# Optimization experiments

Measured on AMD Instinct MI355X. Metric: run time of the kernel, lower is better.

## Reference

```python
import jax, jax.numpy as jnp
import numpy as np

CH = 128; HEADS = 4; HD = CH // HEADS; L = 4; G = 16; NPG = 1024
N = G * NPG; E = 524288; IN_DIM = 64; BN_EPS = 1e-5


def setup_inputs() -> dict:
    key = jax.random.key(0)
    ks = iter(jax.random.split(key, 64))
    def nrm(shape, scale):
        return jax.random.normal(next(ks), shape, dtype=jnp.float32) * scale
    inp = {}
    inp['x'] = jax.random.normal(next(ks), (N, IN_DIM), dtype=jnp.float32)
    inp['edge_attr'] = jnp.ones((E, 1), dtype=jnp.float32)
    inp['edge_index'] = jax.random.randint(next(ks), (2, E), 0, N)
    inp['batch'] = jnp.repeat(jnp.arange(G), NPG)  # equal-sized graphs, sorted
    # input projections
    inp['node_w'] = nrm((CH, IN_DIM), IN_DIM ** -0.5); inp['node_b'] = nrm((CH,), 0.02)
    inp['edge_w'] = nrm((CH, 1), 1.0); inp['edge_b'] = nrm((CH,), 0.02)
    # per-layer stacked params
    inp['gine_w1'] = nrm((L, CH, CH), CH ** -0.5); inp['gine_b1'] = nrm((L, CH), 0.02)
    inp['gine_w2'] = nrm((L, CH, CH), CH ** -0.5); inp['gine_b2'] = nrm((L, CH), 0.02)
    inp['attn_in_w'] = nrm((L, 3 * CH, CH), CH ** -0.5); inp['attn_in_b'] = nrm((L, 3 * CH), 0.02)
    inp['attn_out_w'] = nrm((L, CH, CH), CH ** -0.5); inp['attn_out_b'] = nrm((L, CH), 0.02)
    inp['mlp_w1'] = nrm((L, 2 * CH, CH), CH ** -0.5); inp['mlp_b1'] = nrm((L, 2 * CH), 0.02)
    inp['mlp_w2'] = nrm((L, CH, 2 * CH), (2 * CH) ** -0.5); inp['mlp_b2'] = nrm((L, CH), 0.02)
    # 3 batch norms per layer (eval mode: running stats)
    inp['bn_g'] = 1.0 + nrm((L, 3, CH), 0.05)
    inp['bn_b'] = nrm((L, 3, CH), 0.05)
    inp['bn_m'] = nrm((L, 3, CH), 0.05)
    inp['bn_v'] = 0.5 + jax.random.uniform(next(ks), (L, 3, CH), dtype=jnp.float32)
    # head MLP 128 -> 64 -> 32 -> 1
    inp['head_w1'] = nrm((64, CH), CH ** -0.5); inp['head_b1'] = nrm((64,), 0.02)
    inp['head_w2'] = nrm((32, 64), 64 ** -0.5); inp['head_b2'] = nrm((32,), 0.02)
    inp['head_w3'] = nrm((1, 32), 32 ** -0.5); inp['head_b3'] = nrm((1,), 0.02)
    return inp


def _bn(h, g, b, m, v):
    return (h - m) * jax.lax.rsqrt(v + BN_EPS) * g + b


def _mha(x, in_w, in_b, out_w, out_b):
    # x: [G, NPG, CH]; torch.nn.MultiheadAttention self-attention, no padding (full graphs)
    qkv = x @ in_w.T + in_b
    q, k, v = jnp.split(qkv, 3, axis=-1)
    split = lambda t: t.reshape(G, NPG, HEADS, HD).transpose(0, 2, 1, 3)
    q, k, v = split(q), split(k), split(v)
    scores = jnp.einsum('ghid,ghjd->ghij', q, k) / jnp.sqrt(jnp.float32(HD))
    a = jax.nn.softmax(scores, axis=-1)
    o = jnp.einsum('ghij,ghjd->ghid', a, v).transpose(0, 2, 1, 3).reshape(G, NPG, CH)
    return o @ out_w.T + out_b


def reference(x, edge_attr, edge_index, batch, node_w, node_b, edge_w, edge_b,
              gine_w1, gine_b1, gine_w2, gine_b2,
              attn_in_w, attn_in_b, attn_out_w, attn_out_b,
              mlp_w1, mlp_b1, mlp_w2, mlp_b2,
              bn_g, bn_b, bn_m, bn_v,
              head_w1, head_b1, head_w2, head_b2, head_w3, head_b3):
    h = x @ node_w.T + node_b                      # [N, CH]
    e = edge_attr @ edge_w.T + edge_b              # [E, CH]
    src, dst = edge_index[0], edge_index[1]
    for l in range(L):
        # --- GINEConv: nn((1+eps)*x_i + sum_j relu(x_j + e_ji)), eps=0 ---
        msg = jax.nn.relu(h[src] + e)
        agg = jax.ops.segment_sum(msg, dst, num_segments=N)
        z = h + agg
        z = jax.nn.relu(z @ gine_w1[l].T + gine_b1[l]) @ gine_w2[l].T + gine_b2[l]
        h1 = _bn(z + h, bn_g[l, 0], bn_b[l, 0], bn_m[l, 0], bn_v[l, 0])
        # --- global multihead attention on dense batch of x ---
        a = _mha(h.reshape(G, NPG, CH), attn_in_w[l], attn_in_b[l],
                 attn_out_w[l], attn_out_b[l]).reshape(N, CH)
        h2 = _bn(a + h, bn_g[l, 1], bn_b[l, 1], bn_m[l, 1], bn_v[l, 1])
        # --- combine + FFN (GPSConv mlp: CH -> 2CH -> CH) ---
        out = h1 + h2
        ff = jax.nn.relu(out @ mlp_w1[l].T + mlp_b1[l]) @ mlp_w2[l].T + mlp_b2[l]
        h = _bn(out + ff, bn_g[l, 2], bn_b[l, 2], bn_m[l, 2], bn_v[l, 2])
    # global_add_pool + head MLP
    g = jax.ops.segment_sum(h, batch, num_segments=G)
    g = jax.nn.relu(g @ head_w1.T + head_b1)
    g = jax.nn.relu(g @ head_w2.T + head_b2)
    return g @ head_w3.T + head_b3
```

## Files before the change

### kernel.cpp

```cpp
#include <hip/hip_runtime.h>
#include <hip/hip_bf16.h>

typedef __attribute__((ext_vector_type(8))) short short8;
typedef __attribute__((ext_vector_type(4))) float f32x4;
typedef __attribute__((ext_vector_type(2))) unsigned int u32x2;
typedef unsigned short u16;
typedef unsigned int u32;
typedef unsigned long long u64;

#define NODES 16384
#define CHN 128
#define NEDGE 524288
#define NG 16
#define NPGC 1024
#define NHEAD 4
#define HDIM 32
#define NLAYER 4
#define CL 0.2550348281f

#if __has_builtin(__builtin_amdgcn_exp2f)
#define EXP2(x) __builtin_amdgcn_exp2f(x)
#else
#define EXP2(x) exp2f(x)
#endif

__device__ __forceinline__ float bf2f(u16 u) {
    union { u32 u; float f; } c; c.u = ((u32)u) << 16; return c.f;
}
__device__ __forceinline__ u16 f2bf(float f) {
    union { float f; u32 u; } c; c.f = f;
    u32 r = c.u + 0x7fffu + ((c.u >> 16) & 1u);
    return (u16)(r >> 16);
}
__device__ __forceinline__ void fsplit(float f, u16& hi, u16& lo) {
    u16 h = f2bf(f);
    hi = h;
    lo = f2bf(f - bf2f(h));
}
__device__ __forceinline__ u32 cvtpk_bf16(float a, float b) {
    u32 r;
    asm("v_cvt_pk_bf16_f32 %0, %1, %2" : "=v"(r) : "v"(a), "v"(b));
    return r;
}

#define MFMA16(a, b, c) __builtin_amdgcn_mfma_f32_16x16x32_bf16((a), (b), (c), 0, 0, 0)

__device__ __forceinline__ short8 ld_frag(const u16* p) {
    return *reinterpret_cast<const short8*>(p);
}


struct SplitJobs {
    const float* src[8];
    u16* hi[8];
    u16* lo[8];
    int blk_end[8];
};

__global__ void k_split8(SplitJobs jobs) {
    int b = blockIdx.x;
    int seg = 0;
    while (b >= jobs.blk_end[seg]) ++seg;
    int base = seg ? jobs.blk_end[seg - 1] : 0;
    int i = (b - base) * 256 + threadIdx.x;
    u16 h, l;
    fsplit(jobs.src[seg][i], h, l);
    jobs.hi[seg][i] = h;
    jobs.lo[seg][i] = l;
}

__global__ void k_bnprep(const float* __restrict__ g, const float* __restrict__ b,
                         const float* __restrict__ m, const float* __restrict__ v,
                         float* __restrict__ scale, float* __restrict__ shift) {
    int i = blockIdx.x * 256 + threadIdx.x;
    if (i < NLAYER * 3 * CHN) {
        float s = g[i] * rsqrtf(v[i] + 1e-5f);
        scale[i] = s;
        shift[i] = b[i] - m[i] * s;
    }
}

__global__ void k_zero_u32(u32* __restrict__ p, int n) {
    int i = blockIdx.x * 256 + threadIdx.x;
    if (i < n) p[i] = 0u;
}

__global__ void k_count(const int* __restrict__ dst, u32* __restrict__ counts) {
    int e = blockIdx.x * 256 + threadIdx.x;
    if (e < NEDGE) atomicAdd(&counts[dst[e]], 1u);
}

__global__ void k_scan(const u32* __restrict__ counts, u32* __restrict__ offsets,
                       u32* __restrict__ cursor) {
    __shared__ u32 part[256];
    int t = threadIdx.x;
    int base = t * 64;
    u32 s = 0;
    for (int i = 0; i < 64; ++i) s += counts[base + i];
    part[t] = s;
    __syncthreads();
    for (int off = 1; off < 256; off <<= 1) {
        u32 val = (t >= off) ? part[t - off] : 0u;
        __syncthreads();
        part[t] += val;
        __syncthreads();
    }
    u32 run = (t == 0) ? 0u : part[t - 1];
    for (int i = 0; i < 64; ++i) {
        offsets[base + i] = run;
        cursor[base + i] = run;
        run += counts[base + i];
    }
    if (t == 255) offsets[NODES] = run;
}

__global__ void k_fill(const int* __restrict__ src, const int* __restrict__ dst,
                       const float* __restrict__ eattr, u32* __restrict__ cursor,
                       int2* __restrict__ csr_sa) {
    int e = blockIdx.x * 256 + threadIdx.x;
    if (e >= NEDGE) return;
    int d = dst[e];
    u32 p = atomicAdd(&cursor[d], 1u);
    csr_sa[p] = make_int2(src[e], __float_as_int(eattr[e]));
}


__global__ __launch_bounds__(256) void k_aggqkv(
    const u16* __restrict__ h_hi, const float* __restrict__ h_f32,
    const u32* __restrict__ offsets, const int2* __restrict__ csr_sa,
    const float* __restrict__ ew, const float* __restrict__ eb,
    u16* __restrict__ z_hi, u16* __restrict__ z_lo,
    const u16* __restrict__ h_lo, const u16* __restrict__ Whi,
    const u16* __restrict__ Wlo, const float* __restrict__ bias,
    u16* __restrict__ q_hi, u16* __restrict__ q_lo,
    u16* __restrict__ k_hi, u16* __restrict__ k_lo,
    u16* __restrict__ vt_hi) {
    int tid = threadIdx.x;
    int wave = tid >> 6, lane = tid & 63;
    if (blockIdx.x < NODES / 4) {
        int node = blockIdx.x * 4 + wave;
        int c0 = lane * 2;
        float w0 = ew[c0], w1 = ew[c0 + 1];
        float b0 = eb[c0], b1 = eb[c0 + 1];
        u32 beg = offsets[node], end = offsets[node + 1];
        float acc0 = 0.f, acc1 = 0.f;
        u32 i = beg;
        for (; i + 8 <= end; i += 8) {
            int2 es[8];
            u32 us[8];
#pragma unroll
            for (int j = 0; j < 8; ++j) es[j] = csr_sa[i + j];
#pragma unroll
            for (int j = 0; j < 8; ++j)
                us[j] = *reinterpret_cast<const u32*>(
                    h_hi + (size_t)es[j].x * CHN + c0);
#pragma unroll
            for (int j = 0; j < 8; ++j) {
                float a = __int_as_float(es[j].y);
                float f0 = bf2f((u16)(us[j] & 0xffffu));
                float f1 = bf2f((u16)(us[j] >> 16));
                acc0 += fmaxf(f0 + a * w0 + b0, 0.f);
                acc1 += fmaxf(f1 + a * w1 + b1, 0.f);
            }
        }
        for (; i < end; ++i) {
            int2 e = csr_sa[i];
            u32 u = *reinterpret_cast<const u32*>(h_hi + (size_t)e.x * CHN + c0);
            float a = __int_as_float(e.y);
            float f0 = bf2f((u16)(u & 0xffffu));
            float f1 = bf2f((u16)(u >> 16));
            acc0 += fmaxf(f0 + a * w0 + b0, 0.f);
            acc1 += fmaxf(f1 + a * w1 + b1, 0.f);
        }
        size_t idx = (size_t)node * CHN + c0;
        float z0 = h_f32[idx] + acc0;
        float z1v = h_f32[idx + 1] + acc1;
        u16 h, l;
        fsplit(z0, h, l); z_hi[idx] = h; z_lo[idx] = l;
        fsplit(z1v, h, l); z_hi[idx + 1] = h; z_lo[idx + 1] = l;
        return;
    }
    const int K = 128;
    int id = blockIdx.x - NODES / 4;
    int bx = id & 255, ny = id >> 8;
    int lr = lane & 15, lg = lane >> 4;
    int r0 = bx * 64 + wave * 16;
    int nb = ny * 32;
    f32x4 acc[2] = {};
    size_t arow = (size_t)(r0 + lr) * K + lg * 8;
    for (int ks = 0; ks < K; ks += 32) {
        short8 ah = ld_frag(h_hi + arow + ks);
        short8 al = ld_frag(h_lo + arow + ks);
#pragma unroll
        for (int n = 0; n < 2; ++n) {
            size_t wrow = (size_t)(nb + n * 16 + lr) * K + ks + lg * 8;
            short8 wh = ld_frag(Whi + wrow);
            short8 wl = ld_frag(Wlo + wrow);
            acc[n] = MFMA16(ah, wh, acc[n]);
            acc[n] = MFMA16(al, wh, acc[n]);
            acc[n] = MFMA16(ah, wl, acc[n]);
        }
    }
#pragma unroll
    for (int n = 0; n < 2; ++n) {
        int col = nb + n * 16 + lr;
        int region = col >> 7;
        int c = col & 127;
        int hh = c >> 5, d = c & 31;
        float bs = bias[col];
#pragma unroll
        for (int r = 0; r < 4; ++r) {
            int row = r0 + lg * 4 + r;
            float v = acc[n][r] + bs;
            int g = row >> 10, p = row & 1023;
            size_t gh = (size_t)(g * NHEAD + hh);
            if (region == 0) {
                u16 vh, vl;
                fsplit(v * CL, vh, vl);
                size_t o = (gh * NPGC + p) * HDIM + d;
                q_hi[o] = vh; q_lo[o] = vl;
            } else if (region == 1) {
                u16 vh, vl;
                fsplit(v, vh, vl);
                size_t o = (gh * NPGC + p) * HDIM + d;
                k_hi[o] = vh; k_lo[o] = vl;
            } else {
                vt_hi[(gh * HDIM + d) * NPGC + p] = f2bf(v);
            }
        }
    }
}


__global__ __launch_bounds__(256) void k_gemm(
    const u16* __restrict__ Ahi, const u16* __restrict__ Alo,
    const u16* __restrict__ Whi, const u16* __restrict__ Wlo,
    const float* __restrict__ bias, float* __restrict__ out_f32,
    u16* __restrict__ out_hi, u16* __restrict__ out_lo, int K, int Nc) {
    int tid = threadIdx.x;
    int wave = tid >> 6, lane = tid & 63;
    int lr = lane & 15, lg = lane >> 4;
    int r0 = blockIdx.x * 64 + wave * 16;
    int nb = blockIdx.y * 32;
    f32x4 acc[2] = {};
    size_t arow = (size_t)(r0 + lr) * K + lg * 8;
    for (int ks = 0; ks < K; ks += 32) {
        short8 ah = ld_frag(Ahi + arow + ks);
        short8 al = ld_frag(Alo + arow + ks);
#pragma unroll
        for (int n = 0; n < 2; ++n) {
            size_t wrow = (size_t)(nb + n * 16 + lr) * K + ks + lg * 8;
            short8 wh = ld_frag(Whi + wrow);
            short8 wl = ld_frag(Wlo + wrow);
            acc[n] = MFMA16(ah, wh, acc[n]);
            acc[n] = MFMA16(al, wh, acc[n]);
            acc[n] = MFMA16(ah, wl, acc[n]);
        }
    }
#pragma unroll
    for (int n = 0; n < 2; ++n) {
        int col = nb + n * 16 + lr;
        float bs = bias[col];
#pragma unroll
        for (int r = 0; r < 4; ++r) {
            int row = r0 + lg * 4 + r;
            size_t oidx = (size_t)row * Nc + col;
            float v = acc[n][r] + bs;
            out_f32[oidx] = v;
            u16 hh, ll;
            fsplit(v, hh, ll);
            out_hi[oidx] = hh; out_lo[oidx] = ll;
        }
    }
}


__global__ __launch_bounds__(256) void k_gineattn(
    const u16* __restrict__ zhi, const u16* __restrict__ zlo,
    const u16* __restrict__ w1hi, const u16* __restrict__ w1lo,
    const float* __restrict__ b1,
    const u16* __restrict__ w2hi, const u16* __restrict__ w2lo,
    const float* __restrict__ b2, const float* __restrict__ resid,
    const float* __restrict__ bnsc, const float* __restrict__ bnsh,
    float* __restrict__ h1out,
    const u16* __restrict__ qhi, const u16* __restrict__ qlo,
    const u16* __restrict__ khi, const u16* __restrict__ klo,
    const u16* __restrict__ vthi,
    u16* __restrict__ aohi, u16* __restrict__ aolo) {
    __shared__ __align__(16) u16 smem[64][136];
    int tid = threadIdx.x;
    int wave = tid >> 6, lane = tid & 63;
    int lr = lane & 15, lg = lane >> 4;
    if (blockIdx.x < NODES / 32) {
        int r0 = blockIdx.x * 32;
        int cb = wave * 32;
        {
            f32x4 acc[2][2] = {};
            size_t arow0 = (size_t)(r0 + lr) * CHN + lg * 8;
            size_t arow1 = (size_t)(r0 + 16 + lr) * CHN + lg * 8;
            for (int ks = 0; ks < CHN; ks += 32) {
                short8 ah0 = ld_frag(zhi + arow0 + ks);
                short8 al0 = ld_frag(zlo + arow0 + ks);
                short8 ah1 = ld_frag(zhi + arow1 + ks);
                short8 al1 = ld_frag(zlo + arow1 + ks);
#pragma unroll
                for (int n = 0; n < 2; ++n) {
                    size_t wrow = (size_t)(cb + n * 16 + lr) * CHN + ks + lg * 8;
                    short8 wh = ld_frag(w1hi + wrow);
                    short8 wl = ld_frag(w1lo + wrow);
                    acc[0][n] = MFMA16(ah0, wh, acc[0][n]);
                    acc[0][n] = MFMA16(al0, wh, acc[0][n]);
                    acc[0][n] = MFMA16(ah0, wl, acc[0][n]);
                    acc[1][n] = MFMA16(ah1, wh, acc[1][n]);
                    acc[1][n] = MFMA16(al1, wh, acc[1][n]);
                    acc[1][n] = MFMA16(ah1, wl, acc[1][n]);
                }
            }
#pragma unroll
            for (int rg = 0; rg < 2; ++rg)
#pragma unroll
                for (int n = 0; n < 2; ++n) {
                    int col = cb + n * 16 + lr;
                    float bs = b1[col];
#pragma unroll
                    for (int r = 0; r < 4; ++r) {
                        float v = fmaxf(acc[rg][n][r] + bs, 0.f);
                        u16 hh, ll;
                        fsplit(v, hh, ll);
                        int rl = rg * 16 + lg * 4 + r;
                        smem[rl][col] = hh;
                        smem[32 + rl][col] = ll;
                    }
                }
        }
        __syncthreads();
        {
            f32x4 acc[2][2] = {};
            for (int ks = 0; ks < CHN; ks += 32) {
                short8 ah0 = ld_frag(&smem[lr][ks + lg * 8]);
                short8 al0 = ld_frag(&smem[32 + lr][ks + lg * 8]);
                short8 ah1 = ld_frag(&smem[16 + lr][ks + lg * 8]);
                short8 al1 = ld_frag(&smem[48 + lr][ks + lg * 8]);
#pragma unroll
                for (int n = 0; n < 2; ++n) {
                    size_t wrow = (size_t)(cb + n * 16 + lr) * CHN + ks + lg * 8;
                    short8 wh = ld_frag(w2hi + wrow);
                    short8 wl = ld_frag(w2lo + wrow);
                    acc[0][n] = MFMA16(ah0, wh, acc[0][n]);
                    acc[0][n] = MFMA16(al0, wh, acc[0][n]);
                    acc[0][n] = MFMA16(ah0, wl, acc[0][n]);
                    acc[1][n] = MFMA16(ah1, wh, acc[1][n]);
                    acc[1][n] = MFMA16(al1, wh, acc[1][n]);
                    acc[1][n] = MFMA16(ah1, wl, acc[1][n]);
                }
            }
#pragma unroll
            for (int rg = 0; rg < 2; ++rg)
#pragma unroll
                for (int n = 0; n < 2; ++n) {
                    int col = cb + n * 16 + lr;
                    float bs = b2[col], sc = bnsc[col], sh = bnsh[col];
#pragma unroll
                    for (int r = 0; r < 4; ++r) {
                        int row = r0 + rg * 16 + lg * 4 + r;
                        size_t oidx = (size_t)row * CHN + col;
                        float v = acc[rg][n][r] + bs + resid[oidx];
                        h1out[oidx] = v * sc + sh;
                    }
                }
        }
        return;
    }
    int id = blockIdx.x - NODES / 32;
    int gh = id & 63;
    int bx = id >> 6;
    int qA = bx * 128 + wave * 32;
    int qB = qA + 16;
    size_t base = (size_t)gh * NPGC * HDIM;
    size_t vbase = (size_t)gh * HDIM * NPGC;
    short8 qhA = ld_frag(qhi + base + (size_t)(qA + lr) * HDIM + lg * 8);
    short8 qlA = ld_frag(qlo + base + (size_t)(qA + lr) * HDIM + lg * 8);
    short8 qhB = ld_frag(qhi + base + (size_t)(qB + lr) * HDIM + lg * 8);
    short8 qlB = ld_frag(qlo + base + (size_t)(qB + lr) * HDIM + lg * 8);
    const u16* Kh = khi + base;
    const u16* Kl = klo + base;
    const u16* Vh = vthi + vbase;
    f32x4 o0A = {}, o1A = {}, o0B = {}, o1B = {};
    f32x4 lsA = {}, lsB = {};
    float mA = -1e30f, mB = -1e30f;
    const f32x4 zero = {};
    u16 (*plds)[136] = &smem[wave * 16];
    for (int kv = 0; kv < NPGC; kv += 128) {
        f32x4 sA[8], sB[8];
        __builtin_amdgcn_s_setprio(1);
#pragma unroll
        for (int f = 0; f < 8; ++f) {
            size_t kr = (size_t)(kv + f * 16 + lr) * HDIM + lg * 8;
            short8 kh = ld_frag(Kh + kr);
            short8 kl2 = ld_frag(Kl + kr);
            sA[f] = MFMA16(kh, qlA, MFMA16(kl2, qhA, MFMA16(kh, qhA, zero)));
            sB[f] = MFMA16(kh, qlB, MFMA16(kl2, qhB, MFMA16(kh, qhB, zero)));
        }
        __builtin_amdgcn_s_setprio(0);
        {
            f32x4 mm = sA[0];
#pragma unroll
            for (int f = 1; f < 8; ++f)
#pragma unroll
                for (int i = 0; i < 4; ++i) mm[i] = fmaxf(mm[i], sA[f][i]);
            float mx = fmaxf(fmaxf(mm[0], mm[1]), fmaxf(mm[2], mm[3]));
            if (!__all(mx <= mA + 8.f)) {
                mx = fmaxf(mx, __shfl_xor(mx, 16));
                mx = fmaxf(mx, __shfl_xor(mx, 32));
                float mn = fmaxf(mA, mx);
                float corr = EXP2(mA - mn);
                mA = mn;
#pragma unroll
                for (int i = 0; i < 4; ++i) {
                    lsA[i] *= corr;
                    o0A[i] *= corr; o1A[i] *= corr;
                }
            }
#pragma unroll
            for (int f = 0; f < 8; ++f)
#pragma unroll
                for (int i = 0; i < 4; ++i) sA[f][i] = EXP2(sA[f][i] - mA);
            f32x4 s4 = sA[0];
#pragma unroll
            for (int f = 1; f < 8; ++f)
#pragma unroll
                for (int i = 0; i < 4; ++i) s4[i] += sA[f][i];
            lsA += s4;
#pragma unroll
            for (int f = 0; f < 8; ++f) {
                u32x2 wv;
                wv[0] = cvtpk_bf16(sA[f][0], sA[f][1]);
                wv[1] = cvtpk_bf16(sA[f][2], sA[f][3]);
                *reinterpret_cast<u32x2*>(&plds[lr][f * 16 + lg * 4]) = wv;
            }
        }
        short8 vs0[4], vs1[4];
        __builtin_amdgcn_s_setprio(1);
#pragma unroll
        for (int kk = 0; kk < 4; ++kk) {
            short8 pf = ld_frag(&plds[lr][kk * 32 + lg * 8]);
            vs0[kk] = ld_frag(Vh + (size_t)lr * NPGC + kv + kk * 32 + lg * 8);
            vs1[kk] = ld_frag(Vh + (size_t)(16 + lr) * NPGC + kv + kk * 32 + lg * 8);
            o0A = MFMA16(vs0[kk], pf, o0A);
            o1A = MFMA16(vs1[kk], pf, o1A);
        }
        __builtin_amdgcn_s_setprio(0);
        {
            f32x4 mm = sB[0];
#pragma unroll
            for (int f = 1; f < 8; ++f)
#pragma unroll
                for (int i = 0; i < 4; ++i) mm[i] = fmaxf(mm[i], sB[f][i]);
            float mx = fmaxf(fmaxf(mm[0], mm[1]), fmaxf(mm[2], mm[3]));
            if (!__all(mx <= mB + 8.f)) {
                mx = fmaxf(mx, __shfl_xor(mx, 16));
                mx = fmaxf(mx, __shfl_xor(mx, 32));
                float mn = fmaxf(mB, mx);
                float corr = EXP2(mB - mn);
                mB = mn;
#pragma unroll
                for (int i = 0; i < 4; ++i) {
                    lsB[i] *= corr;
                    o0B[i] *= corr; o1B[i] *= corr;
                }
            }
#pragma unroll
            for (int f = 0; f < 8; ++f)
#pragma unroll
                for (int i = 0; i < 4; ++i) sB[f][i] = EXP2(sB[f][i] - mB);
            f32x4 s4 = sB[0];
#pragma unroll
            for (int f = 1; f < 8; ++f)
#pragma unroll
                for (int i = 0; i < 4; ++i) s4[i] += sB[f][i];
            lsB += s4;
#pragma unroll
            for (int f = 0; f < 8; ++f) {
                u32x2 wv;
                wv[0] = cvtpk_bf16(sB[f][0], sB[f][1]);
                wv[1] = cvtpk_bf16(sB[f][2], sB[f][3]);
                *reinterpret_cast<u32x2*>(&plds[lr][f * 16 + lg * 4]) = wv;
            }
        }
        __builtin_amdgcn_s_setprio(1);
#pragma unroll
        for (int kk = 0; kk < 4; ++kk) {
            short8 pf = ld_frag(&plds[lr][kk * 32 + lg * 8]);
            o0B = MFMA16(vs0[kk], pf, o0B);
            o1B = MFMA16(vs1[kk], pf, o1B);
        }
        __builtin_amdgcn_s_setprio(0);
    }
    float lA = (lsA[0] + lsA[1]) + (lsA[2] + lsA[3]);
    lA += __shfl_xor(lA, 16);
    lA += __shfl_xor(lA, 32);
    float lB = (lsB[0] + lsB[1]) + (lsB[2] + lsB[3]);
    lB += __shfl_xor(lB, 16);
    lB += __shfl_xor(lB, 32);
    int g = gh >> 2, hh = gh & 3;
    {
        float inv = 1.f / lA;
        size_t obase = ((size_t)g * NPGC + qA + lr) * CHN + hh * HDIM;
        union { u16 u[4]; u64 v; } p0h, p0l, p1h, p1l;
#pragma unroll
        for (int i = 0; i < 4; ++i) {
            u16 a, b;
            fsplit(o0A[i] * inv, a, b); p0h.u[i] = a; p0l.u[i] = b;
            fsplit(o1A[i] * inv, a, b); p1h.u[i] = a; p1l.u[i] = b;
        }
        *reinterpret_cast<u64*>(aohi + obase + lg * 4) = p0h.v;
        *reinterpret_cast<u64*>(aolo + obase + lg * 4) = p0l.v;
        *reinterpret_cast<u64*>(aohi + obase + 16 + lg * 4) = p1h.v;
        *reinterpret_cast<u64*>(aolo + obase + 16 + lg * 4) = p1l.v;
    }
    {
        float inv = 1.f / lB;
        size_t obase = ((size_t)g * NPGC + qB + lr) * CHN + hh * HDIM;
        union { u16 u[4]; u64 v; } p0h, p0l, p1h, p1l;
#pragma unroll
        for (int i = 0; i < 4; ++i) {
            u16 a, b;
            fsplit(o0B[i] * inv, a, b); p0h.u[i] = a; p0l.u[i] = b;
            fsplit(o1B[i] * inv, a, b); p1h.u[i] = a; p1l.u[i] = b;
        }
        *reinterpret_cast<u64*>(aohi + obase + lg * 4) = p0h.v;
        *reinterpret_cast<u64*>(aolo + obase + lg * 4) = p0l.v;
        *reinterpret_cast<u64*>(aohi + obase + 16 + lg * 4) = p1h.v;
        *reinterpret_cast<u64*>(aolo + obase + 16 + lg * 4) = p1l.v;
    }
}


__global__ __launch_bounds__(256) void k_outffn(
    const u16* __restrict__ aoh, const u16* __restrict__ aol,
    const u16* __restrict__ awh, const u16* __restrict__ awl,
    const float* __restrict__ ab, const float* __restrict__ hres,
    const float* __restrict__ sc1, const float* __restrict__ sh1,
    const float* __restrict__ h1res,
    const u16* __restrict__ w1h, const u16* __restrict__ w1l,
    const float* __restrict__ b1,
    const u16* __restrict__ w2h, const u16* __restrict__ w2l,
    const float* __restrict__ b2,
    const float* __restrict__ sc2, const float* __restrict__ sh2,
    float* __restrict__ hf, u16* __restrict__ hhi, u16* __restrict__ hlo) {
    __shared__ __align__(16) u16 o_hi[32][136];
    __shared__ __align__(16) u16 o_lo[32][136];
    __shared__ __align__(16) u16 t_hi[32][264];
    __shared__ __align__(16) u16 t_lo[32][264];
    int tid = threadIdx.x;
    int wave = tid >> 6, lane = tid & 63;
    int lr = lane & 15, lg = lane >> 4;
    int r0 = blockIdx.x * 32;
    int cb = wave * 32;
    {
        f32x4 acc[2][2] = {};
        size_t arow0 = (size_t)(r0 + lr) * CHN + lg * 8;
        size_t arow1 = (size_t)(r0 + 16 + lr) * CHN + lg * 8;
        for (int ks = 0; ks < CHN; ks += 32) {
            short8 ah0 = ld_frag(aoh + arow0 + ks);
            short8 al0 = ld_frag(aol + arow0 + ks);
            short8 ah1 = ld_frag(aoh + arow1 + ks);
            short8 al1 = ld_frag(aol + arow1 + ks);
#pragma unroll
            for (int n = 0; n < 2; ++n) {
                size_t wrow = (size_t)(cb + n * 16 + lr) * CHN + ks + lg * 8;
                short8 wh = ld_frag(awh + wrow);
                short8 wl = ld_frag(awl + wrow);
                acc[0][n] = MFMA16(ah0, wh, acc[0][n]);
                acc[0][n] = MFMA16(al0, wh, acc[0][n]);
                acc[0][n] = MFMA16(ah0, wl, acc[0][n]);
                acc[1][n] = MFMA16(ah1, wh, acc[1][n]);
                acc[1][n] = MFMA16(al1, wh, acc[1][n]);
                acc[1][n] = MFMA16(ah1, wl, acc[1][n]);
            }
        }
#pragma unroll
        for (int rg = 0; rg < 2; ++rg)
#pragma unroll
            for (int n = 0; n < 2; ++n) {
                int col = cb + n * 16 + lr;
                float bs = ab[col], sc = sc1[col], sh = sh1[col];
#pragma unroll
                for (int r = 0; r < 4; ++r) {
                    int row = r0 + rg * 16 + lg * 4 + r;
                    int rl = rg * 16 + lg * 4 + r;
                    size_t oidx = (size_t)row * CHN + col;
                    float v = (acc[rg][n][r] + bs + hres[oidx]) * sc + sh + h1res[oidx];
                    u16 hh, ll;
                    fsplit(v, hh, ll);
                    o_hi[rl][col] = hh; o_lo[rl][col] = ll;
                }
            }
    }
    __syncthreads();
    {
        f32x4 acc[2][4] = {};
        int cbB = wave * 64;
        for (int ks = 0; ks < CHN; ks += 32) {
            short8 ah0 = ld_frag(&o_hi[lr][ks + lg * 8]);
            short8 al0 = ld_frag(&o_lo[lr][ks + lg * 8]);
            short8 ah1 = ld_frag(&o_hi[16 + lr][ks + lg * 8]);
            short8 al1 = ld_frag(&o_lo[16 + lr][ks + lg * 8]);
#pragma unroll
            for (int n = 0; n < 4; ++n) {
                size_t wrow = (size_t)(cbB + n * 16 + lr) * CHN + ks + lg * 8;
                short8 wh = ld_frag(w1h + wrow);
                short8 wl = ld_frag(w1l + wrow);
                acc[0][n] = MFMA16(ah0, wh, acc[0][n]);
                acc[0][n] = MFMA16(al0, wh, acc[0][n]);
                acc[0][n] = MFMA16(ah0, wl, acc[0][n]);
                acc[1][n] = MFMA16(ah1, wh, acc[1][n]);
                acc[1][n] = MFMA16(al1, wh, acc[1][n]);
                acc[1][n] = MFMA16(ah1, wl, acc[1][n]);
            }
        }
#pragma unroll
        for (int rg = 0; rg < 2; ++rg)
#pragma unroll
            for (int n = 0; n < 4; ++n) {
                int col = cbB + n * 16 + lr;
                float bs = b1[col];
#pragma unroll
                for (int r = 0; r < 4; ++r) {
                    float v = fmaxf(acc[rg][n][r] + bs, 0.f);
                    u16 hh, ll;
                    fsplit(v, hh, ll);
                    int rl = rg * 16 + lg * 4 + r;
                    t_hi[rl][col] = hh;
                    t_lo[rl][col] = ll;
                }
            }
    }
    __syncthreads();
    {
        f32x4 acc[2][2] = {};
        for (int ks = 0; ks < 2 * CHN; ks += 32) {
            short8 ah0 = ld_frag(&t_hi[lr][ks + lg * 8]);
            short8 al0 = ld_frag(&t_lo[lr][ks + lg * 8]);
            short8 ah1 = ld_frag(&t_hi[16 + lr][ks + lg * 8]);
            short8 al1 = ld_frag(&t_lo[16 + lr][ks + lg * 8]);
#pragma unroll
            for (int n = 0; n < 2; ++n) {
                size_t wrow = (size_t)(cb + n * 16 + lr) * 2 * CHN + ks + lg * 8;
                short8 wh = ld_frag(w2h + wrow);
                short8 wl = ld_frag(w2l + wrow);
                acc[0][n] = MFMA16(ah0, wh, acc[0][n]);
                acc[0][n] = MFMA16(al0, wh, acc[0][n]);
                acc[0][n] = MFMA16(ah0, wl, acc[0][n]);
                acc[1][n] = MFMA16(ah1, wh, acc[1][n]);
                acc[1][n] = MFMA16(al1, wh, acc[1][n]);
                acc[1][n] = MFMA16(ah1, wl, acc[1][n]);
            }
        }
#pragma unroll
        for (int rg = 0; rg < 2; ++rg)
#pragma unroll
            for (int n = 0; n < 2; ++n) {
                int col = cb + n * 16 + lr;
                float bs = b2[col], sc = sc2[col], sh = sh2[col];
#pragma unroll
                for (int r = 0; r < 4; ++r) {
                    int row = r0 + rg * 16 + lg * 4 + r;
                    int rl = rg * 16 + lg * 4 + r;
                    size_t oidx = (size_t)row * CHN + col;
                    float ores = bf2f(o_hi[rl][col]) + bf2f(o_lo[rl][col]);
                    float v = (acc[rg][n][r] + bs + ores) * sc + sh;
                    hf[oidx] = v;
                    u16 hh, ll;
                    fsplit(v, hh, ll);
                    hhi[oidx] = hh; hlo[oidx] = ll;
                }
            }
    }
}


__global__ __launch_bounds__(128) void k_pool(const float* __restrict__ h,
                                              float* __restrict__ pool) {
    int g = blockIdx.x, sl = blockIdx.y, c = threadIdx.x;
    const float* p = h + ((size_t)g * NPGC + sl * 128) * CHN + c;
    float s = 0.f;
    for (int i = 0; i < 128; ++i) s += p[(size_t)i * CHN];
    atomicAdd(&pool[g * CHN + c], s);
}

__global__ __launch_bounds__(256) void k_head(
    const float* __restrict__ pool, const float* __restrict__ w1,
    const float* __restrict__ b1, const float* __restrict__ w2,
    const float* __restrict__ b2, const float* __restrict__ w3,
    const float* __restrict__ b3, float* __restrict__ out) {
    __shared__ float g1[16][64];
    __shared__ float g2[16][32];
    int t = threadIdx.x;
    for (int idx = t; idx < 16 * 64; idx += 256) {
        int g = idx >> 6, n = idx & 63;
        float s = b1[n];
        for (int k = 0; k < 128; ++k) s += pool[g * 128 + k] * w1[n * 128 + k];
        g1[g][n] = fmaxf(s, 0.f);
    }
    __syncthreads();
    for (int idx = t; idx < 16 * 32; idx += 256) {
        int g = idx >> 5, n = idx & 31;
        float s = b2[n];
        for (int k = 0; k < 64; ++k) s += g1[g][k] * w2[n * 64 + k];
        g2[g][n] = fmaxf(s, 0.f);
    }
    __syncthreads();
    if (t < 16) {
        float s = b3[0];
        for (int k = 0; k < 32; ++k) s += g2[t][k] * w3[k];
        out[t] = s;
    }
}


extern "C" void kernel_launch(void* const* d_in, const int* in_sizes, int n_in,
                              void* d_out, int out_size, void* d_ws, size_t ws_size,
                              hipStream_t stream) {
    (void)in_sizes; (void)n_in; (void)out_size; (void)ws_size;
    const float* x = (const float*)d_in[0];
    const float* edge_attr = (const float*)d_in[1];
    const int* edge_index = (const int*)d_in[2];
    const float* node_w = (const float*)d_in[4];
    const float* node_b = (const float*)d_in[5];
    const float* edge_w = (const float*)d_in[6];
    const float* edge_b = (const float*)d_in[7];
    const float* gine_w1 = (const float*)d_in[8];
    const float* gine_b1 = (const float*)d_in[9];
    const float* gine_w2 = (const float*)d_in[10];
    const float* gine_b2 = (const float*)d_in[11];
    const float* attn_in_w = (const float*)d_in[12];
    const float* attn_in_b = (const float*)d_in[13];
    const float* attn_out_w = (const float*)d_in[14];
    const float* attn_out_b = (const float*)d_in[15];
    const float* mlp_w1 = (const float*)d_in[16];
    const float* mlp_b1 = (const float*)d_in[17];
    const float* mlp_w2 = (const float*)d_in[18];
    const float* mlp_b2 = (const float*)d_in[19];
    const float* bn_g = (const float*)d_in[20];
    const float* bn_bb = (const float*)d_in[21];
    const float* bn_m = (const float*)d_in[22];
    const float* bn_v = (const float*)d_in[23];
    const float* head_w1 = (const float*)d_in[24];
    const float* head_b1 = (const float*)d_in[25];
    const float* head_w2 = (const float*)d_in[26];
    const float* head_b2 = (const float*)d_in[27];
    const float* head_w3 = (const float*)d_in[28];
    const float* head_b3 = (const float*)d_in[29];

    char* ws = (char*)d_ws;
    size_t off = 0;
    auto alloc = [&](size_t bytes) {
        size_t r = off;
        off = (off + bytes + 255) & ~(size_t)255;
        return r;
    };
    const size_t NC = (size_t)NODES * CHN;
    float* h_f32 = (float*)(ws + alloc(NC * 4));
    u16* h_hi = (u16*)(ws + alloc(NC * 2));
    u16* h_lo = (u16*)(ws + alloc(NC * 2));
    u16* x_hi = (u16*)(ws + alloc((size_t)NODES * 64 * 2));
    u16* x_lo = (u16*)(ws + alloc((size_t)NODES * 64 * 2));
    u16* zao_hi = (u16*)(ws + alloc(NC * 2));
    u16* zao_lo = (u16*)(ws + alloc(NC * 2));
    float* h1_f32 = (float*)(ws + alloc(NC * 4));
    u16* q_hi = (u16*)(ws + alloc(NC * 2));
    u16* q_lo = (u16*)(ws + alloc(NC * 2));
    u16* kk_hi = (u16*)(ws + alloc(NC * 2));
    u16* kk_lo = (u16*)(ws + alloc(NC * 2));
    u16* vt_hi = (u16*)(ws + alloc(NC * 2));
    float* pool = (float*)(ws + alloc(NG * CHN * 4));
    u16* node_w_hi = (u16*)(ws + alloc(CHN * 64 * 2));
    u16* node_w_lo = (u16*)(ws + alloc(CHN * 64 * 2));
    u16* gw1_hi = (u16*)(ws + alloc((size_t)NLAYER * CHN * CHN * 2));
    u16* gw1_lo = (u16*)(ws + alloc((size_t)NLAYER * CHN * CHN * 2));
    u16* gw2_hi = (u16*)(ws + alloc((size_t)NLAYER * CHN * CHN * 2));
    u16* gw2_lo = (u16*)(ws + alloc((size_t)NLAYER * CHN * CHN * 2));
    u16* aiw_hi = (u16*)(ws + alloc((size_t)NLAYER * 3 * CHN * CHN * 2));
    u16* aiw_lo = (u16*)(ws + alloc((size_t)NLAYER * 3 * CHN * CHN * 2));
    u16* aow_hi = (u16*)(ws + alloc((size_t)NLAYER * CHN * CHN * 2));
    u16* aow_lo = (u16*)(ws + alloc((size_t)NLAYER * CHN * CHN * 2));
    u16* mw1_hi = (u16*)(ws + alloc((size_t)NLAYER * 2 * CHN * CHN * 2));
    u16* mw1_lo = (u16*)(ws + alloc((size_t)NLAYER * 2 * CHN * CHN * 2));
    u16* mw2_hi = (u16*)(ws + alloc((size_t)NLAYER * 2 * CHN * CHN * 2));
    u16* mw2_lo = (u16*)(ws + alloc((size_t)NLAYER * 2 * CHN * CHN * 2));
    float* bn_scale = (float*)(ws + alloc(NLAYER * 3 * CHN * 4));
    float* bn_shift = (float*)(ws + alloc(NLAYER * 3 * CHN * 4));
    u32* counts = (u32*)(ws + alloc(NODES * 4));
    u32* offsets = (u32*)(ws + alloc((NODES + 1) * 4));
    u32* cursor = (u32*)(ws + alloc(NODES * 4));
    int2* csr_sa = (int2*)(ws + alloc((size_t)NEDGE * 8));

    const int* e_src = edge_index;
    const int* e_dst = edge_index + NEDGE;

    {
        SplitJobs j;
        const float* srcs[8] = {x, node_w, gine_w1, gine_w2, attn_in_w,
                                attn_out_w, mlp_w1, mlp_w2};
        u16* his[8] = {x_hi, node_w_hi, gw1_hi, gw2_hi, aiw_hi, aow_hi, mw1_hi, mw2_hi};
        u16* los[8] = {x_lo, node_w_lo, gw1_lo, gw2_lo, aiw_lo, aow_lo, mw1_lo, mw2_lo};
        int ns[8] = {NODES * 64, CHN * 64, NLAYER * CHN * CHN, NLAYER * CHN * CHN,
                     NLAYER * 3 * CHN * CHN, NLAYER * CHN * CHN,
                     NLAYER * 2 * CHN * CHN, NLAYER * 2 * CHN * CHN};
        int cum = 0;
        for (int i = 0; i < 8; ++i) {
            j.src[i] = srcs[i]; j.hi[i] = his[i]; j.lo[i] = los[i];
            cum += ns[i] / 256;
            j.blk_end[i] = cum;
        }
        k_split8<<<dim3(cum), dim3(256), 0, stream>>>(j);
    }

    k_bnprep<<<dim3((NLAYER * 3 * CHN + 255) / 256), dim3(256), 0, stream>>>(
        bn_g, bn_bb, bn_m, bn_v, bn_scale, bn_shift);

    k_zero_u32<<<dim3(NODES / 256), dim3(256), 0, stream>>>(counts, NODES);
    k_count<<<dim3(NEDGE / 256), dim3(256), 0, stream>>>(e_dst, counts);
    k_scan<<<dim3(1), dim3(256), 0, stream>>>(counts, offsets, cursor);
    k_fill<<<dim3(NEDGE / 256), dim3(256), 0, stream>>>(e_src, e_dst, edge_attr,
                                                        cursor, csr_sa);

    k_gemm<<<dim3(NODES / 64, CHN / 32), dim3(256), 0, stream>>>(
        x_hi, x_lo, node_w_hi, node_w_lo, node_b, h_f32, h_hi, h_lo, 64, CHN);

    for (int l = 0; l < NLAYER; ++l) {
        size_t wo = (size_t)l * CHN * CHN;
        const float* sc0 = bn_scale + (l * 3 + 0) * CHN;
        const float* sh0 = bn_shift + (l * 3 + 0) * CHN;
        const float* sc1 = bn_scale + (l * 3 + 1) * CHN;
        const float* sh1 = bn_shift + (l * 3 + 1) * CHN;
        const float* sc2 = bn_scale + (l * 3 + 2) * CHN;
        const float* sh2 = bn_shift + (l * 3 + 2) * CHN;

        k_aggqkv<<<dim3(NODES / 4 + 3072), dim3(256), 0, stream>>>(
            h_hi, h_f32, offsets, csr_sa, edge_w, edge_b, zao_hi, zao_lo,
            h_lo, aiw_hi + wo * 3, aiw_lo + wo * 3, attn_in_b + l * 3 * CHN,
            q_hi, q_lo, kk_hi, kk_lo, vt_hi);
        k_gineattn<<<dim3(NODES / 32 + 512), dim3(256), 0, stream>>>(
            zao_hi, zao_lo, gw1_hi + wo, gw1_lo + wo, gine_b1 + l * CHN,
            gw2_hi + wo, gw2_lo + wo, gine_b2 + l * CHN, h_f32, sc0, sh0, h1_f32,
            q_hi, q_lo, kk_hi, kk_lo, vt_hi, zao_hi, zao_lo);
        k_outffn<<<dim3(NODES / 32), dim3(256), 0, stream>>>(
            zao_hi, zao_lo, aow_hi + wo, aow_lo + wo, attn_out_b + l * CHN,
            h_f32, sc1, sh1, h1_f32,
            mw1_hi + wo * 2, mw1_lo + wo * 2, mlp_b1 + l * 2 * CHN,
            mw2_hi + wo * 2, mw2_lo + wo * 2, mlp_b2 + l * CHN, sc2, sh2,
            h_f32, h_hi, h_lo);
    }

    k_zero_u32<<<dim3(NG * CHN / 256), dim3(256), 0, stream>>>((u32*)pool, NG * CHN);
    k_pool<<<dim3(NG, 8), dim3(128), 0, stream>>>(h_f32, pool);
    k_head<<<dim3(1), dim3(256), 0, stream>>>(pool, head_w1, head_b1, head_w2,
                                              head_b2, head_w3, head_b3,
                                              (float*)d_out);
}
```

Before: 688.7 us.

## Split edge aggregation across two waves per node and enlarge GINE MLP row tiles

The aggregation part of k_aggqkv now assigns two waves per node, each summing half of the node's edge list with 16 gathers in flight and predicated tails, then combines the partial sums through shared memory. This is meant to expose more memory-level parallelism for the latency-bound gather. Separately, the GINE MLP blocks in k_gineattn now process 64 rows instead of 32, so each weight fragment is reused across more rows. The cost is more registers, double the shared memory in that kernel, and a block-wide barrier in the aggregation path.

```diff
diff --git a/kernel.cpp b/kernel.cpp
--- a/kernel.cpp
+++ b/kernel.cpp
@@ -135,53 +135,64 @@
     u16* __restrict__ q_hi, u16* __restrict__ q_lo,
     u16* __restrict__ k_hi, u16* __restrict__ k_lo,
     u16* __restrict__ vt_hi) {
+    __shared__ float psum[2][128];
     int tid = threadIdx.x;
     int wave = tid >> 6, lane = tid & 63;
-    if (blockIdx.x < NODES / 4) {
-        int node = blockIdx.x * 4 + wave;
+    if (blockIdx.x < NODES / 2) {
+        int nl = wave >> 1;
+        int sub = wave & 1;
+        int node = blockIdx.x * 2 + nl;
         int c0 = lane * 2;
         float w0 = ew[c0], w1 = ew[c0 + 1];
         float b0 = eb[c0], b1 = eb[c0 + 1];
-        u32 beg = offsets[node], end = offsets[node + 1];
+        u32 beg0 = offsets[node], end0 = offsets[node + 1];
+        u32 mid = (beg0 + end0) >> 1;
+        u32 beg = sub ? mid : beg0;
+        u32 end = sub ? end0 : mid;
         float acc0 = 0.f, acc1 = 0.f;
-        u32 i = beg;
-        for (; i + 8 <= end; i += 8) {
-            int2 es[8];
-            u32 us[8];
-#pragma unroll
-            for (int j = 0; j < 8; ++j) es[j] = csr_sa[i + j];
-#pragma unroll
-            for (int j = 0; j < 8; ++j)
+        for (u32 i = beg; i < end; i += 16) {
+            int2 es[16];
+            u32 us[16];
+#pragma unroll
+            for (int j = 0; j < 16; ++j) {
+                u32 jj = i + j;
+                jj = jj < end ? jj : end - 1;
+                es[j] = csr_sa[jj];
+            }
+#pragma unroll
+            for (int j = 0; j < 16; ++j)
                 us[j] = *reinterpret_cast<const u32*>(
                     h_hi + (size_t)es[j].x * CHN + c0);
 #pragma unroll
-            for (int j = 0; j < 8; ++j) {
-                float a = __int_as_float(es[j].y);
-                float f0 = bf2f((u16)(us[j] & 0xffffu));
-                float f1 = bf2f((u16)(us[j] >> 16));
-                acc0 += fmaxf(f0 + a * w0 + b0, 0.f);
-                acc1 += fmaxf(f1 + a * w1 + b1, 0.f);
-            }
-        }
-        for (; i < end; ++i) {
-            int2 e = csr_sa[i];
-            u32 u = *reinterpret_cast<const u32*>(h_hi + (size_t)e.x * CHN + c0);
-            float a = __int_as_float(e.y);
-            float f0 = bf2f((u16)(u & 0xffffu));
-            float f1 = bf2f((u16)(u >> 16));
-            acc0 += fmaxf(f0 + a * w0 + b0, 0.f);
-            acc1 += fmaxf(f1 + a * w1 + b1, 0.f);
-        }
-        size_t idx = (size_t)node * CHN + c0;
-        float z0 = h_f32[idx] + acc0;
-        float z1v = h_f32[idx + 1] + acc1;
-        u16 h, l;
-        fsplit(z0, h, l); z_hi[idx] = h; z_lo[idx] = l;
-        fsplit(z1v, h, l); z_hi[idx + 1] = h; z_lo[idx + 1] = l;
+            for (int j = 0; j < 16; ++j) {
+                if (i + j < end) {
+                    float a = __int_as_float(es[j].y);
+                    float f0 = bf2f((u16)(us[j] & 0xffffu));
+                    float f1 = bf2f((u16)(us[j] >> 16));
+                    acc0 += fmaxf(f0 + a * w0 + b0, 0.f);
+                    acc1 += fmaxf(f1 + a * w1 + b1, 0.f);
+                }
+            }
+        }
+        if (sub) {
+            psum[nl][c0] = acc0;
+            psum[nl][c0 + 1] = acc1;
+        }
+        __syncthreads();
+        if (!sub) {
+            acc0 += psum[nl][c0];
+            acc1 += psum[nl][c0 + 1];
+            size_t idx = (size_t)node * CHN + c0;
+            float z0 = h_f32[idx] + acc0;
+            float z1v = h_f32[idx + 1] + acc1;
+            u16 h, l;
+            fsplit(z0, h, l); z_hi[idx] = h; z_lo[idx] = l;
+            fsplit(z1v, h, l); z_hi[idx + 1] = h; z_lo[idx + 1] = l;
+        }
         return;
     }
     const int K = 128;
-    int id = blockIdx.x - NODES / 4;
+    int id = blockIdx.x - NODES / 2;
     int bx = id & 255, ny = id >> 8;
     int lr = lane & 15, lg = lane >> 4;
     int r0 = bx * 64 + wave * 16;
@@ -287,37 +298,38 @@
     const u16* __restrict__ khi, const u16* __restrict__ klo,
     const u16* __restrict__ vthi,
     u16* __restrict__ aohi, u16* __restrict__ aolo) {
-    __shared__ __align__(16) u16 smem[64][136];
+    __shared__ __align__(16) u16 smem[128][136];
     int tid = threadIdx.x;
     int wave = tid >> 6, lane = tid & 63;
     int lr = lane & 15, lg = lane >> 4;
-    if (blockIdx.x < NODES / 32) {
-        int r0 = blockIdx.x * 32;
+    if (blockIdx.x < NODES / 64) {
+        int r0 = blockIdx.x * 64;
         int cb = wave * 32;
         {
-            f32x4 acc[2][2] = {};
-            size_t arow0 = (size_t)(r0 + lr) * CHN + lg * 8;
-            size_t arow1 = (size_t)(r0 + 16 + lr) * CHN + lg * 8;
+            f32x4 acc[4][2] = {};
             for (int ks = 0; ks < CHN; ks += 32) {
-                short8 ah0 = ld_frag(zhi + arow0 + ks);
-                short8 al0 = ld_frag(zlo + arow0 + ks);
-                short8 ah1 = ld_frag(zhi + arow1 + ks);
-                short8 al1 = ld_frag(zlo + arow1 + ks);
+                short8 ah[4], al[4];
+#pragma unroll
+                for (int rg = 0; rg < 4; ++rg) {
+                    size_t arow = (size_t)(r0 + rg * 16 + lr) * CHN + ks + lg * 8;
+                    ah[rg] = ld_frag(zhi + arow);
+                    al[rg] = ld_frag(zlo + arow);
+                }
 #pragma unroll
                 for (int n = 0; n < 2; ++n) {
                     size_t wrow = (size_t)(cb + n * 16 + lr) * CHN + ks + lg * 8;
                     short8 wh = ld_frag(w1hi + wrow);
                     short8 wl = ld_frag(w1lo + wrow);
-                    acc[0][n] = MFMA16(ah0, wh, acc[0][n]);
-                    acc[0][n] = MFMA16(al0, wh, acc[0][n]);
-                    acc[0][n] = MFMA16(ah0, wl, acc[0][n]);
-                    acc[1][n] = MFMA16(ah1, wh, acc[1][n]);
-                    acc[1][n] = MFMA16(al1, wh, acc[1][n]);
-                    acc[1][n] = MFMA16(ah1, wl, acc[1][n]);
-                }
-            }
-#pragma unroll
-            for (int rg = 0; rg < 2; ++rg)
+#pragma unroll
+                    for (int rg = 0; rg < 4; ++rg) {
+                        acc[rg][n] = MFMA16(ah[rg], wh, acc[rg][n]);
+                        acc[rg][n] = MFMA16(al[rg], wh, acc[rg][n]);
+                        acc[rg][n] = MFMA16(ah[rg], wl, acc[rg][n]);
+                    }
+                }
+            }
+#pragma unroll
+            for (int rg = 0; rg < 4; ++rg)
 #pragma unroll
                 for (int n = 0; n < 2; ++n) {
                     int col = cb + n * 16 + lr;
@@ -329,33 +341,35 @@
                         fsplit(v, hh, ll);
                         int rl = rg * 16 + lg * 4 + r;
                         smem[rl][col] = hh;
-                        smem[32 + rl][col] = ll;
+                        smem[64 + rl][col] = ll;
                     }
                 }
         }
         __syncthreads();
         {
-            f32x4 acc[2][2] = {};
+            f32x4 acc[4][2] = {};
             for (int ks = 0; ks < CHN; ks += 32) {
-                short8 ah0 = ld_frag(&smem[lr][ks + lg * 8]);
-                short8 al0 = ld_frag(&smem[32 + lr][ks + lg * 8]);
-                short8 ah1 = ld_frag(&smem[16 + lr][ks + lg * 8]);
-                short8 al1 = ld_frag(&smem[48 + lr][ks + lg * 8]);
+                short8 ah[4], al[4];
+#pragma unroll
+                for (int rg = 0; rg < 4; ++rg) {
+                    ah[rg] = ld_frag(&smem[rg * 16 + lr][ks + lg * 8]);
+                    al[rg] = ld_frag(&smem[64 + rg * 16 + lr][ks + lg * 8]);
+                }
 #pragma unroll
                 for (int n = 0; n < 2; ++n) {
                     size_t wrow = (size_t)(cb + n * 16 + lr) * CHN + ks + lg * 8;
                     short8 wh = ld_frag(w2hi + wrow);
                     short8 wl = ld_frag(w2lo + wrow);
-                    acc[0][n] = MFMA16(ah0, wh, acc[0][n]);
-                    acc[0][n] = MFMA16(al0, wh, acc[0][n]);
-                    acc[0][n] = MFMA16(ah0, wl, acc[0][n]);
-                    acc[1][n] = MFMA16(ah1, wh, acc[1][n]);
-                    acc[1][n] = MFMA16(al1, wh, acc[1][n]);
-                    acc[1][n] = MFMA16(ah1, wl, acc[1][n]);
-                }
-            }
-#pragma unroll
-            for (int rg = 0; rg < 2; ++rg)
+#pragma unroll
+                    for (int rg = 0; rg < 4; ++rg) {
+                        acc[rg][n] = MFMA16(ah[rg], wh, acc[rg][n]);
+                        acc[rg][n] = MFMA16(al[rg], wh, acc[rg][n]);
+                        acc[rg][n] = MFMA16(ah[rg], wl, acc[rg][n]);
+                    }
+                }
+            }
+#pragma unroll
+            for (int rg = 0; rg < 4; ++rg)
 #pragma unroll
                 for (int n = 0; n < 2; ++n) {
                     int col = cb + n * 16 + lr;
@@ -371,7 +385,7 @@
         }
         return;
     }
-    int id = blockIdx.x - NODES / 32;
+    int id = blockIdx.x - NODES / 64;
     int gh = id & 63;
     int bx = id >> 6;
     int qA = bx * 128 + wave * 32;
@@ -838,11 +852,11 @@
         const float* sc2 = bn_scale + (l * 3 + 2) * CHN;
         const float* sh2 = bn_shift + (l * 3 + 2) * CHN;
 
-        k_aggqkv<<<dim3(NODES / 4 + 3072), dim3(256), 0, stream>>>(
+        k_aggqkv<<<dim3(NODES / 2 + 3072), dim3(256), 0, stream>>>(
             h_hi, h_f32, offsets, csr_sa, edge_w, edge_b, zao_hi, zao_lo,
             h_lo, aiw_hi + wo * 3, aiw_lo + wo * 3, attn_in_b + l * 3 * CHN,
             q_hi, q_lo, kk_hi, kk_lo, vt_hi);
-        k_gineattn<<<dim3(NODES / 32 + 512), dim3(256), 0, stream>>>(
+        k_gineattn<<<dim3(NODES / 64 + 512), dim3(256), 0, stream>>>(
             zao_hi, zao_lo, gw1_hi + wo, gw1_lo + wo, gine_b1 + l * CHN,
             gw2_hi + wo, gw2_lo + wo, gine_b2 + l * CHN, h_f32, sc0, sh0, h1_f32,
             q_hi, q_lo, kk_hi, kk_lo, vt_hi, zao_hi, zao_lo);
```

Result: slower. 713.2 us (+3.6%).
